# Kernel tuning notes

Hardware: AMD Instinct MI355X
Metric: run time of the kernel (lower is better)

Reference implementation:

```python
import jax, jax.numpy as jnp
import numpy as np

D = 128; H = 8; DH = D // H
N = 50000; B = 8; MAXN = N // B
E = 400000
NG_G = 4; NG_L = 4; NG = NG_G + NG_L
DFF = 2 * D


def _ln(x, eps=1e-5):
    m = x.mean(-1, keepdims=True)
    v = ((x - m) ** 2).mean(-1, keepdims=True)
    return (x - m) * jax.lax.rsqrt(v + eps)


def _mha(q, k, v, in_w, in_b, out_w, out_b):
    # torch nn.MultiheadAttention (batch_first, eval) with packed in_proj
    Bq, Lq, d = q.shape; Lk = k.shape[1]
    wq, wk, wv = jnp.split(in_w, 3, axis=0)
    bq, bk, bv = jnp.split(in_b, 3)
    Q = (q @ wq.T + bq).reshape(Bq, Lq, H, DH).transpose(0, 2, 1, 3)
    K = (k @ wk.T + bk).reshape(Bq, Lk, H, DH).transpose(0, 2, 1, 3)
    V = (v @ wv.T + bv).reshape(Bq, Lk, H, DH).transpose(0, 2, 1, 3)
    A = jax.nn.softmax(jnp.einsum('bhqd,bhkd->bhqk', Q, K) / np.float32(np.sqrt(DH)), axis=-1)
    O = jnp.einsum('bhqk,bhkd->bhqd', A, V).transpose(0, 2, 1, 3).reshape(Bq, Lq, d)
    return O @ out_w.T + out_b, A.mean(axis=1)  # averaged attn weights over heads


def _tconv(x, src, dst, Wq, bq, Wk, bk, Wv, bv, Wskip, bskip, Wbeta):
    # PyG TransformerConv(d, d//H, heads=H, beta=True): edge-wise gather-attend-scatter
    n = x.shape[0]
    q = (x @ Wq.T + bq)[dst].reshape(-1, H, DH)   # [E,H,DH] query at target node
    k = (x @ Wk.T + bk)[src].reshape(-1, H, DH)
    v = (x @ Wv.T + bv)[src].reshape(-1, H, DH)
    logits = (q * k).sum(-1) / np.float32(np.sqrt(DH))  # [E,H]
    m = jax.ops.segment_max(logits, dst, num_segments=n)
    m = jnp.where(jnp.isfinite(m), m, 0.0)
    a = jnp.exp(logits - m[dst])
    s = jax.ops.segment_sum(a, dst, num_segments=n)
    alpha = a / (s[dst] + 1e-16)                  # per-target-node softmax (PyG softmax)
    out = jax.ops.segment_sum(v * alpha[..., None], dst, num_segments=n).reshape(n, D)
    xr = x @ Wskip.T + bskip                      # root weight
    beta = jax.nn.sigmoid(jnp.concatenate([out, xr, out - xr], axis=-1) @ Wbeta.T)
    return beta * xr + (1.0 - beta) * out


def setup_inputs() -> dict:
    key = jax.random.key(0)
    ks = jax.random.split(key, 16)
    w = lambda i, shape, s=0.05: jax.random.normal(ks[i], shape, jnp.float32) * s
    return dict(
        x=w(0, (N, D), 1.0),
        edge_index=jax.random.randint(ks[1], (2, E), 0, N),
        global_h=w(2, (B, NG, D), 1.0),
        batch=jnp.repeat(jnp.arange(B, dtype=jnp.int32), MAXN),  # sorted, even split
        n_global_tokens_global=NG_G,
        n_global_tokens_local=NG_L,
        Wq=w(3, (D, D)), bq=jnp.zeros((D,), jnp.float32),
        Wk=w(4, (D, D)), bk=jnp.zeros((D,), jnp.float32),
        Wv=w(5, (D, D)), bv=jnp.zeros((D,), jnp.float32),
        Wskip=w(6, (D, D)), bskip=jnp.zeros((D,), jnp.float32),
        Wbeta=w(7, (1, 3 * D)),
        ng_in_w=w(8, (3 * D, D)), ng_in_b=jnp.zeros((3 * D,), jnp.float32),
        ng_out_w=w(9, (D, D)), ng_out_b=jnp.zeros((D,), jnp.float32),
        gn_in_w=w(10, (3 * D, D)), gn_in_b=jnp.zeros((3 * D,), jnp.float32),
        gn_out_w=w(11, (D, D)), gn_out_b=jnp.zeros((D,), jnp.float32),
        W1=w(12, (DFF, D)), b1=jnp.zeros((DFF,), jnp.float32),
        W2=w(13, (D, DFF)), b2=jnp.zeros((D,), jnp.float32),
    )


def reference(x, edge_index, global_h, batch, n_global_tokens_global, n_global_tokens_local,
              Wq, bq, Wk, bk, Wv, bv, Wskip, bskip, Wbeta,
              ng_in_w, ng_in_b, ng_out_w, ng_out_b,
              gn_in_w, gn_in_b, gn_out_w, gn_out_b,
              W1, b1, W2, b2):
    src, dst = edge_index[0], edge_index[1]
    h_local = _tconv(x, src, dst, Wq, bq, Wk, bk, Wv, bv, Wskip, bskip, Wbeta)
    x = _ln(x + h_local)
    Bg = global_h.shape[0]
    # to_dense_batch: batch is sorted with equal-size graphs -> mask all True, pure reshape
    dense_x = x.reshape(Bg, -1, D)
    global_out, attn_w = _mha(global_h, dense_x, dense_x, ng_in_w, ng_in_b, ng_out_w, ng_out_b)
    global_h = _ln(global_h + global_out)
    nodes_out, _ = _mha(dense_x, global_h, global_h, gn_in_w, gn_in_b, gn_out_w, gn_out_b)
    dense_x = _ln(dense_x + nodes_out)
    x = dense_x.reshape(-1, D)  # un-scatter (even split -> reshape)
    ff = jax.nn.relu(x @ W1.T + b1) @ W2.T + b2
    x = _ln(x + ff)
    # attention regularization, vectorized over the per-graph python loop
    ls = n_global_tokens_global
    le = ls + n_global_tokens_local
    P = attn_w[:, ls:le, :]                      # [B, K, max_n], all nodes valid
    Pn = P / (P.sum(-1, keepdims=True) + 1e-8)
    G = jnp.einsum('bkn,bmn->bkm', Pn, Pn)       # [B, K, K]
    Kt = le - ls
    off = (G.sum(axis=(1, 2)) - jnp.einsum('bkk->b', G)) / (Kt * Kt - Kt)
    reg = off.mean()
    return x, global_h, reg
```

## Files before the change

kernel.cpp:

```cpp
#include <hip/hip_runtime.h>
#include <math.h>

#define D 128
#define H 8
#define NGT 8
#define LSTOK 4

typedef short bf16x8 __attribute__((ext_vector_type(8)));
typedef float f32x4  __attribute__((ext_vector_type(4)));

__device__ __forceinline__ short f2bf(float f) {
  union { float f; unsigned u; } v; v.f = f;
  unsigned r = v.u + 0x7FFFu + ((v.u >> 16) & 1u);
  return (short)(r >> 16);
}
__device__ __forceinline__ float bf2f(short s) {
  union { unsigned u; float f; } v;
  v.u = ((unsigned)(unsigned short)s) << 16;
  return v.f;
}
__device__ __forceinline__ float4 bf4(bf16x8 v, int lo) {
  return make_float4(bf2f(v[lo]), bf2f(v[lo + 1]), bf2f(v[lo + 2]), bf2f(v[lo + 3]));
}
__device__ __forceinline__ unsigned pk2(float a, float b) {
  return ((unsigned)(unsigned short)f2bf(b) << 16) | (unsigned short)f2bf(a);
}

__device__ __forceinline__ float dot4(float4 a, float4 b) {
  return a.x*b.x + a.y*b.y + a.z*b.z + a.w*b.w;
}
__device__ __forceinline__ float4 scale_madd(float4 a, float sc, float4 v, float p) {
  return make_float4(fmaf(p, v.x, a.x*sc), fmaf(p, v.y, a.y*sc),
                     fmaf(p, v.z, a.z*sc), fmaf(p, v.w, a.w*sc));
}
__device__ __forceinline__ float4 comb4(float4 a, float e1, float4 c, float e2) {
  return make_float4(a.x*e1 + c.x*e2, a.y*e1 + c.y*e2, a.z*e1 + c.z*e2, a.w*e1 + c.w*e2);
}
__device__ __forceinline__ float4 shfl_xor4(float4 v, int off) {
  return make_float4(__shfl_xor(v.x, off), __shfl_xor(v.y, off),
                     __shfl_xor(v.z, off), __shfl_xor(v.w, off));
}

struct CvtArgs {
  const float* s[10];
  short*       d[10];
  int          n[10];
};

__global__ void cvt_weights(CvtArgs a) {
  int which = blockIdx.y;
  const float* s = a.s[which];
  short* d = a.d[which];
  int n = a.n[which];
  int i = (blockIdx.x * 256 + threadIdx.x) * 4;
  if (i + 3 < n) {
    float4 v = *(const float4*)(s + i);
    d[i]     = f2bf(v.x);
    d[i + 1] = f2bf(v.y);
    d[i + 2] = f2bf(v.z);
    d[i + 3] = f2bf(v.w);
  }
}

__global__ void cvt_x(const float* __restrict__ s, short* __restrict__ d, int n) {
  int i = (blockIdx.x * 256 + threadIdx.x) * 8;
  if (i + 7 < n) {
    float4 a = *(const float4*)(s + i);
    float4 b = *(const float4*)(s + i + 4);
    bf16x8 v;
    v[0] = f2bf(a.x); v[1] = f2bf(a.y); v[2] = f2bf(a.z); v[3] = f2bf(a.w);
    v[4] = f2bf(b.x); v[5] = f2bf(b.y); v[6] = f2bf(b.z); v[7] = f2bf(b.w);
    *(bf16x8*)(d + i) = v;
  }
}

__global__ void concat_bias4(const float* __restrict__ b0, const float* __restrict__ b1,
                             const float* __restrict__ b2, const float* __restrict__ b3,
                             float* __restrict__ out) {
  int t = threadIdx.x;
  out[t] = b0[t]; out[128 + t] = b1[t]; out[256 + t] = b2[t]; out[384 + t] = b3[t];
}

#define EPST 72
template<int K>
__global__ void __launch_bounds__(256) gemm_direct(const short* __restrict__ A,
    const short* __restrict__ Wb, const float* __restrict__ bias,
    short* __restrict__ out16, int C16, int s16,
    float* __restrict__ out32, int s32,
    int Nrows, int Ccols, int relu)
{
  __shared__ short eplds[4][64 * EPST];
  const int t = threadIdx.x;
  const int wid = t >> 6, lane = t & 63;
  const int rowBase = blockIdx.x * 128 + (wid >> 1) * 64;
  const int colBase = blockIdx.y * 128 + (wid & 1) * 64;
  const int lrow = lane & 15;
  const int lk = (lane >> 4) * 8;

  f32x4 acc[4][4];
  f32x4 z4 = {0.f, 0.f, 0.f, 0.f};
#pragma unroll
  for (int m = 0; m < 4; m++)
#pragma unroll
    for (int n = 0; n < 4; n++) acc[m][n] = z4;

  const short* ap[4];
#pragma unroll
  for (int m = 0; m < 4; ++m) {
    int ar = rowBase + m * 16 + lrow;
    if (ar >= Nrows) ar = Nrows - 1;
    ap[m] = A + (size_t)ar * K + lk;
  }
  const short* wp[4];
#pragma unroll
  for (int n = 0; n < 4; ++n)
    wp[n] = Wb + (size_t)(colBase + n * 16 + lrow) * K + lk;

#pragma unroll
  for (int kb = 0; kb < K; kb += 32) {
    bf16x8 af[4], bfr[4];
#pragma unroll
    for (int m = 0; m < 4; ++m) af[m] = *(const bf16x8*)(ap[m] + kb);
#pragma unroll
    for (int n = 0; n < 4; ++n) bfr[n] = *(const bf16x8*)(wp[n] + kb);
#pragma unroll
    for (int m = 0; m < 4; ++m)
#pragma unroll
      for (int n = 0; n < 4; ++n)
        acc[m][n] = __builtin_amdgcn_mfma_f32_16x16x32_bf16(af[m], bfr[n], acc[m][n], 0, 0, 0);
  }

  const int ccol = lane & 15;
  const int rquad = (lane >> 4) * 4;
  if (colBase < C16) {
    short* lds = eplds[wid];
#pragma unroll
    for (int n = 0; n < 4; ++n) {
      float bb = bias[colBase + n * 16 + ccol];
      int col = n * 16 + ccol;
#pragma unroll
      for (int m = 0; m < 4; ++m) {
        int r0 = m * 16 + rquad;
#pragma unroll
        for (int r = 0; r < 4; ++r) {
          float v = acc[m][n][r] + bb;
          if (relu) v = fmaxf(v, 0.f);
          lds[(r0 + r) * EPST + col] = f2bf(v);
        }
      }
    }
    const int jr = lane >> 3, jc = lane & 7;
#pragma unroll
    for (int i = 0; i < 8; ++i) {
      int row = i * 8 + jr;
      int gr = rowBase + row;
      if (gr < Nrows) {
        bf16x8 v = *(const bf16x8*)(lds + row * EPST + jc * 8);
        *(bf16x8*)(out16 + (size_t)gr * s16 + colBase + jc * 8) = v;
      }
    }
  } else {
#pragma unroll
    for (int n = 0; n < 4; ++n) {
      int col = colBase + n * 16 + ccol;
      float bb = bias[col];
#pragma unroll
      for (int m = 0; m < 4; ++m) {
        int row0 = rowBase + m * 16 + rquad;
#pragma unroll
        for (int r = 0; r < 4; ++r) {
          int gr = row0 + r;
          if (gr < Nrows) {
            float v = acc[m][n][r] + bb;
            if (relu) v = fmaxf(v, 0.f);
            out32[(size_t)gr * s32 + (col - C16)] = v;
          }
        }
      }
    }
  }
}

__global__ void gemm_small(const float* __restrict__ A, const float* __restrict__ W,
                           const float* __restrict__ bias, float* __restrict__ out, int M)
{
  int r = blockIdx.x;
  int c = threadIdx.x;
  __shared__ float as[128];
  as[c] = A[(size_t)r * 128 + c];
  __syncthreads();
  float acc = bias[c];
  const float* wr = W + (size_t)c * 128;
#pragma unroll 4
  for (int k = 0; k < 128; k++) acc += as[k] * wr[k];
  out[(size_t)r * 128 + c] = acc;
}

__global__ void count_deg(const int* __restrict__ dst, int* __restrict__ deg, int E) {
  int e = blockIdx.x * 256 + threadIdx.x;
  if (e < E) atomicAdd(&deg[dst[e]], 1);
}

__global__ void scan_pass1(const int* __restrict__ deg, int* __restrict__ bsum, int N) {
  int t = threadIdx.x, lane = t & 63, wid = t >> 6;
  int idx = blockIdx.x * 1024 + t * 4;
  int4 v = {0, 0, 0, 0};
  if (idx + 3 < N) v = *(const int4*)(deg + idx);
  else {
    if (idx < N) v.x = deg[idx];
    if (idx + 1 < N) v.y = deg[idx + 1];
    if (idx + 2 < N) v.z = deg[idx + 2];
    if (idx + 3 < N) v.w = deg[idx + 3];
  }
  int s = v.x + v.y + v.z + v.w;
#pragma unroll
  for (int off = 32; off >= 1; off >>= 1) s += __shfl_xor(s, off);
  __shared__ int ws[4];
  if (lane == 0) ws[wid] = s;
  __syncthreads();
  if (t == 0) bsum[blockIdx.x] = ws[0] + ws[1] + ws[2] + ws[3];
}

__global__ void scan_pass2(int* __restrict__ bsum, int SB) {
  __shared__ int sh[1024];
  int t = threadIdx.x;
  sh[t] = (t < SB) ? bsum[t] : 0;
  __syncthreads();
  for (int off = 1; off < 1024; off <<= 1) {
    int v = (t >= off) ? sh[t - off] : 0;
    __syncthreads();
    sh[t] += v;
    __syncthreads();
  }
  if (t < SB) bsum[t] = (t == 0) ? 0 : sh[t - 1];
}

__global__ void scan_pass3(const int* __restrict__ deg, const int* __restrict__ bsum,
                           int* __restrict__ row_start, int* __restrict__ cursor,
                           int N, int E)
{
  int t = threadIdx.x, lane = t & 63, wid = t >> 6;
  int idx = blockIdx.x * 1024 + t * 4;
  int4 v = {0, 0, 0, 0};
  if (idx + 3 < N) v = *(const int4*)(deg + idx);
  else {
    if (idx < N) v.x = deg[idx];
    if (idx + 1 < N) v.y = deg[idx + 1];
    if (idx + 2 < N) v.z = deg[idx + 2];
    if (idx + 3 < N) v.w = deg[idx + 3];
  }
  int ts = v.x + v.y + v.z + v.w;
  int x = ts;
#pragma unroll
  for (int off = 1; off < 64; off <<= 1) {
    int y = __shfl_up(x, off);
    if (lane >= off) x += y;
  }
  __shared__ int ws[4];
  if (lane == 63) ws[wid] = x;
  __syncthreads();
  int woff = 0;
  for (int i = 0; i < wid; i++) woff += ws[i];
  int p = bsum[blockIdx.x] + woff + (x - ts);
  if (idx < N)     { row_start[idx] = p; cursor[idx] = p; }     p += v.x;
  if (idx + 1 < N) { row_start[idx + 1] = p; cursor[idx + 1] = p; } p += v.y;
  if (idx + 2 < N) { row_start[idx + 2] = p; cursor[idx + 2] = p; } p += v.z;
  if (idx + 3 < N) { row_start[idx + 3] = p; cursor[idx + 3] = p; }
  if (blockIdx.x == 0 && t == 0) row_start[N] = E;
}

__global__ void fill_edges(const int* __restrict__ dst, int* __restrict__ cursor,
                           int* __restrict__ edge_list, int E) {
  int e = blockIdx.x * 256 + threadIdx.x;
  if (e < E) {
    int p = atomicAdd(&cursor[dst[e]], 1);
    edge_list[p] = e;
  }
}

__global__ void tconv_attn(const short* __restrict__ qkvb,
                           const int* __restrict__ row_start,
                           const int* __restrict__ edge_list, const int* __restrict__ srcI,
                           float* __restrict__ out, int N)
{
  int gid = blockIdx.x * 256 + threadIdx.x;
  if (gid >= N * H) return;
  int n = gid >> 3, h = gid & 7;
  const short* qp = qkvb + (size_t)n * 384 + h * 16;
  bf16x8 qa = *(const bf16x8*)(qp);
  bf16x8 qb = *(const bf16x8*)(qp + 8);
  float4 q0 = bf4(qa, 0), q1 = bf4(qa, 4), q2 = bf4(qb, 0), q3 = bf4(qb, 4);
  float m = -3.0e38f, s = 0.f;
  float4 a0 = make_float4(0, 0, 0, 0), a1 = a0, a2 = a0, a3 = a0;
  int e1 = row_start[n + 1];
  for (int ei = row_start[n]; ei < e1; ei++) {
    int sn = srcI[edge_list[ei]];
    const short* kp = qkvb + (size_t)sn * 384 + 128 + h * 16;
    bf16x8 k0 = *(const bf16x8*)(kp);
    bf16x8 k1 = *(const bf16x8*)(kp + 8);
    float d = dot4(q0, bf4(k0, 0)) + dot4(q1, bf4(k0, 4))
            + dot4(q2, bf4(k1, 0)) + dot4(q3, bf4(k1, 4));
    d *= 0.25f;
    float mn = fmaxf(m, d);
    float sc = expf(m - mn);
    float p = expf(d - mn);
    bf16x8 v0 = *(const bf16x8*)(kp + 128);
    bf16x8 v1 = *(const bf16x8*)(kp + 136);
    a0 = scale_madd(a0, sc, bf4(v0, 0), p);
    a1 = scale_madd(a1, sc, bf4(v0, 4), p);
    a2 = scale_madd(a2, sc, bf4(v1, 0), p);
    a3 = scale_madd(a3, sc, bf4(v1, 4), p);
    s = s * sc + p;
    m = mn;
  }
  float inv = 1.f / (s + 1e-16f);
  float4* o4 = (float4*)(out + (size_t)n * 128 + h * 16);
  o4[0] = make_float4(a0.x * inv, a0.y * inv, a0.z * inv, a0.w * inv);
  o4[1] = make_float4(a1.x * inv, a1.y * inv, a1.z * inv, a1.w * inv);
  o4[2] = make_float4(a2.x * inv, a2.y * inv, a2.z * inv, a2.w * inv);
  o4[3] = make_float4(a3.x * inv, a3.y * inv, a3.z * inv, a3.w * inv);
}

__global__ void gate_ln(const float* __restrict__ x, const float* __restrict__ att,
                        const float* __restrict__ xr32, const float* __restrict__ Wb,
                        float* __restrict__ x1, short* __restrict__ x1b, int N)
{
  int wid = threadIdx.x >> 6, lane = threadIdx.x & 63;
  int n = blockIdx.x * 4 + wid;
  if (n >= N) return;
  size_t base = (size_t)n * 128 + lane * 2;
  float2 o = *(const float2*)(att + base);
  float2 r = *(const float2*)(xr32 + base);
  float2 xv = *(const float2*)(x + base);
  float2 w0 = *(const float2*)(Wb + lane * 2);
  float2 w1 = *(const float2*)(Wb + 128 + lane * 2);
  float2 w2 = *(const float2*)(Wb + 256 + lane * 2);
  float ts = o.x * w0.x + o.y * w0.y + r.x * w1.x + r.y * w1.y
           + (o.x - r.x) * w2.x + (o.y - r.y) * w2.y;
#pragma unroll
  for (int mm = 32; mm >= 1; mm >>= 1) ts += __shfl_xor(ts, mm);
  float beta = 1.f / (1.f + expf(-ts));
  float2 y;
  y.x = xv.x + beta * r.x + (1.f - beta) * o.x;
  y.y = xv.y + beta * r.y + (1.f - beta) * o.y;
  float sm = y.x + y.y;
#pragma unroll
  for (int mm = 32; mm >= 1; mm >>= 1) sm += __shfl_xor(sm, mm);
  float mean = sm * (1.f / 128.f);
  float dx = y.x - mean, dy = y.y - mean;
  float vs = dx * dx + dy * dy;
#pragma unroll
  for (int mm = 32; mm >= 1; mm >>= 1) vs += __shfl_xor(vs, mm);
  float rstd = rsqrtf(vs * (1.f / 128.f) + 1e-5f);
  float ox = dx * rstd, oy = dy * rstd;
  *(float2*)(x1 + base) = make_float2(ox, oy);
  *(unsigned*)(x1b + base) = pk2(ox, oy);
}

__global__ void ln_add(const float* __restrict__ a, const float* __restrict__ b,
                       float* __restrict__ out, short* __restrict__ out16, int R)
{
  int wid = threadIdx.x >> 6, lane = threadIdx.x & 63;
  int r = blockIdx.x * 4 + wid;
  if (r >= R) return;
  size_t base = (size_t)r * 128 + lane * 2;
  float2 av = *(const float2*)(a + base);
  float2 bv = *(const float2*)(b + base);
  float2 y = make_float2(av.x + bv.x, av.y + bv.y);
  float sm = y.x + y.y;
#pragma unroll
  for (int mm = 32; mm >= 1; mm >>= 1) sm += __shfl_xor(sm, mm);
  float mean = sm * (1.f / 128.f);
  float dx = y.x - mean, dy = y.y - mean;
  float vs = dx * dx + dy * dy;
#pragma unroll
  for (int mm = 32; mm >= 1; mm >>= 1) vs += __shfl_xor(vs, mm);
  float rstd = rsqrtf(vs * (1.f / 128.f) + 1e-5f);
  float ox = dx * rstd, oy = dy * rstd;
  *(float2*)(out + base) = make_float2(ox, oy);
  if (out16) *(unsigned*)(out16 + base) = pk2(ox, oy);
}

__global__ void glob_attn(const float* __restrict__ Qg, const short* __restrict__ kv,
                          float* __restrict__ Og,
                          float* __restrict__ m_gl, float* __restrict__ is_gl, int MAXN)
{
  int blk = blockIdx.x;
  int h = blk & 7, g = (blk >> 3) & 7, b = blk >> 6;
  int lane = threadIdx.x;
  const float4* q4 = (const float4*)(Qg + (size_t)(b * NGT + g) * 128 + h * 16);
  float4 q0 = q4[0], q1 = q4[1], q2 = q4[2], q3 = q4[3];
  float m = -3.0e38f, s = 0.f;
  float4 a0 = make_float4(0, 0, 0, 0), a1 = a0, a2 = a0, a3 = a0;
  for (int n = lane; n < MAXN; n += 64) {
    const short* kp = kv + ((size_t)(b * MAXN + n)) * 256 + h * 16;
    bf16x8 k0 = *(const bf16x8*)(kp);
    bf16x8 k1 = *(const bf16x8*)(kp + 8);
    float d = dot4(q0, bf4(k0, 0)) + dot4(q1, bf4(k0, 4))
            + dot4(q2, bf4(k1, 0)) + dot4(q3, bf4(k1, 4));
    d *= 0.25f;
    float mn = fmaxf(m, d);
    float sc = expf(m - mn);
    float p = expf(d - mn);
    bf16x8 v0 = *(const bf16x8*)(kp + 128);
    bf16x8 v1 = *(const bf16x8*)(kp + 136);
    a0 = scale_madd(a0, sc, bf4(v0, 0), p);
    a1 = scale_madd(a1, sc, bf4(v0, 4), p);
    a2 = scale_madd(a2, sc, bf4(v1, 0), p);
    a3 = scale_madd(a3, sc, bf4(v1, 4), p);
    s = s * sc + p;
    m = mn;
  }
#pragma unroll
  for (int off = 32; off >= 1; off >>= 1) {
    float m2 = __shfl_xor(m, off);
    float s2 = __shfl_xor(s, off);
    float4 c0 = shfl_xor4(a0, off), c1 = shfl_xor4(a1, off);
    float4 c2 = shfl_xor4(a2, off), c3 = shfl_xor4(a3, off);
    float mn = fmaxf(m, m2);
    float e1 = expf(m - mn), e2 = expf(m2 - mn);
    s = s * e1 + s2 * e2;
    a0 = comb4(a0, e1, c0, e2);
    a1 = comb4(a1, e1, c1, e2);
    a2 = comb4(a2, e1, c2, e2);
    a3 = comb4(a3, e1, c3, e2);
    m = mn;
  }
  if (lane == 0) {
    float inv = 1.f / s;
    float4* o4 = (float4*)(Og + (size_t)(b * NGT + g) * 128 + h * 16);
    o4[0] = make_float4(a0.x * inv, a0.y * inv, a0.z * inv, a0.w * inv);
    o4[1] = make_float4(a1.x * inv, a1.y * inv, a1.z * inv, a1.w * inv);
    o4[2] = make_float4(a2.x * inv, a2.y * inv, a2.z * inv, a2.w * inv);
    o4[3] = make_float4(a3.x * inv, a3.y * inv, a3.z * inv, a3.w * inv);
    m_gl[blk] = m;
    is_gl[blk] = inv;
  }
}

__global__ void pker(const float* __restrict__ Qg, const short* __restrict__ kv,
                     const float* __restrict__ m_gl, const float* __restrict__ is_gl,
                     float* __restrict__ P, int MAXN)
{
  int nchunk = (MAXN + 255) >> 8;
  int b = blockIdx.x / nchunk;
  int ch = blockIdx.x % nchunk;
  __shared__ float qs[4 * 128];
  __shared__ float ms[32], iss[32];
  for (int i = threadIdx.x; i < 512; i += 256)
    qs[i] = Qg[(size_t)(b * NGT + LSTOK) * 128 + i];
  if (threadIdx.x < 32) {
    int g = threadIdx.x >> 3, h = threadIdx.x & 7;
    ms[threadIdx.x]  = m_gl[(b * NGT + LSTOK + g) * H + h];
    iss[threadIdx.x] = is_gl[(b * NGT + LSTOK + g) * H + h];
  }
  __syncthreads();
  int n = ch * 256 + threadIdx.x;
  if (n >= MAXN) return;
  float acc[4] = {0.f, 0.f, 0.f, 0.f};
  const short* kbase = kv + ((size_t)(b * MAXN + n)) * 256;
  for (int h = 0; h < H; h++) {
    bf16x8 ka = *(const bf16x8*)(kbase + h * 16);
    bf16x8 kb = *(const bf16x8*)(kbase + h * 16 + 8);
    float4 k0 = bf4(ka, 0), k1 = bf4(ka, 4), k2 = bf4(kb, 0), k3 = bf4(kb, 4);
#pragma unroll
    for (int g = 0; g < 4; g++) {
      const float4* qp = (const float4*)(qs + g * 128 + h * 16);
      float d = dot4(k0, qp[0]) + dot4(k1, qp[1]) + dot4(k2, qp[2]) + dot4(k3, qp[3]);
      d *= 0.25f;
      acc[g] += expf(d - ms[g * 8 + h]) * iss[g * 8 + h];
    }
  }
#pragma unroll
  for (int g = 0; g < 4; g++)
    P[(size_t)(b * 4 + g) * MAXN + n] = acc[g] * 0.125f;
}

__global__ void regk(const float* __restrict__ P, float* __restrict__ offb, int MAXN)
{
  int b = blockIdx.x;
  int t = threadIdx.x;
  float v[10];
#pragma unroll
  for (int i = 0; i < 10; i++) v[i] = 0.f;
  for (int n = t; n < MAXN; n += 256) {
    float p0 = P[(size_t)(b * 4 + 0) * MAXN + n];
    float p1 = P[(size_t)(b * 4 + 1) * MAXN + n];
    float p2 = P[(size_t)(b * 4 + 2) * MAXN + n];
    float p3 = P[(size_t)(b * 4 + 3) * MAXN + n];
    v[0] += p0; v[1] += p1; v[2] += p2; v[3] += p3;
    v[4] += p0 * p1; v[5] += p0 * p2; v[6] += p0 * p3;
    v[7] += p1 * p2; v[8] += p1 * p3; v[9] += p2 * p3;
  }
#pragma unroll
  for (int i = 0; i < 10; i++) {
    float x = v[i];
#pragma unroll
    for (int mm = 32; mm >= 1; mm >>= 1) x += __shfl_xor(x, mm);
    v[i] = x;
  }
  __shared__ float red[4][10];
  int wid = t >> 6, lane = t & 63;
  if (lane == 0)
    for (int i = 0; i < 10; i++) red[wid][i] = v[i];
  __syncthreads();
  if (t == 0) {
    float r[10];
    for (int i = 0; i < 10; i++) r[i] = red[0][i] + red[1][i] + red[2][i] + red[3][i];
    float r0 = r[0] + 1e-8f, r1 = r[1] + 1e-8f, r2 = r[2] + 1e-8f, r3 = r[3] + 1e-8f;
    float off = 2.f * (r[4] / (r0 * r1) + r[5] / (r0 * r2) + r[6] / (r0 * r3)
                     + r[7] / (r1 * r2) + r[8] / (r1 * r3) + r[9] / (r2 * r3));
    offb[b] = off * (1.f / 12.f);
  }
}

__global__ void regfin(const float* __restrict__ offb, float* __restrict__ out) {
  if (threadIdx.x == 0 && blockIdx.x == 0) {
    float s = 0.f;
    for (int i = 0; i < 8; i++) s += offb[i];
    *out = s * (1.f / 8.f);
  }
}

__global__ void node_attn(const short* __restrict__ Qn, const float* __restrict__ Kg,
                          const float* __restrict__ Vg, short* __restrict__ On,
                          int N, int MAXN)
{
  __shared__ float kg[2][NGT * 128];
  __shared__ float vg[2][NGT * 128];
  int n0 = blockIdx.x * 32;
  int b0 = n0 / MAXN;
  int nlast = n0 + 31; if (nlast >= N) nlast = N - 1;
  int bLast = nlast / MAXN;
  int nb = (bLast != b0) ? 2 : 1;
  for (int bi = 0; bi < nb; ++bi) {
    size_t gb = (size_t)((b0 + bi) * NGT) * 128;
    int i = threadIdx.x * 4;
    *(float4*)&kg[bi][i] = *(const float4*)(Kg + gb + i);
    *(float4*)&vg[bi][i] = *(const float4*)(Vg + gb + i);
  }
  __syncthreads();
  int n = n0 + (threadIdx.x >> 3), h = threadIdx.x & 7;
  if (n >= N) return;
  int bi = (n / MAXN) - b0;
  const short* qp = Qn + (size_t)n * 128 + h * 16;
  bf16x8 qa = *(const bf16x8*)(qp);
  bf16x8 qb = *(const bf16x8*)(qp + 8);
  float4 q0 = bf4(qa, 0), q1 = bf4(qa, 4), q2 = bf4(qb, 0), q3 = bf4(qb, 4);
  float l[NGT];
  float mx = -3.0e38f;
#pragma unroll
  for (int tk = 0; tk < NGT; tk++) {
    const float4* k4 = (const float4*)(&kg[bi][tk * 128 + h * 16]);
    float d = dot4(q0, k4[0]) + dot4(q1, k4[1]) + dot4(q2, k4[2]) + dot4(q3, k4[3]);
    l[tk] = d * 0.25f;
    mx = fmaxf(mx, l[tk]);
  }
  float s = 0.f;
#pragma unroll
  for (int tk = 0; tk < NGT; tk++) { l[tk] = expf(l[tk] - mx); s += l[tk]; }
  float inv = 1.f / s;
  float4 a0 = make_float4(0, 0, 0, 0), a1 = a0, a2 = a0, a3 = a0;
#pragma unroll
  for (int tk = 0; tk < NGT; tk++) {
    float p = l[tk] * inv;
    const float4* v4 = (const float4*)(&vg[bi][tk * 128 + h * 16]);
    a0 = scale_madd(a0, 1.f, v4[0], p);
    a1 = scale_madd(a1, 1.f, v4[1], p);
    a2 = scale_madd(a2, 1.f, v4[2], p);
    a3 = scale_madd(a3, 1.f, v4[3], p);
  }
  unsigned* o = (unsigned*)(On + (size_t)n * 128 + h * 16);
  o[0] = pk2(a0.x, a0.y); o[1] = pk2(a0.z, a0.w);
  o[2] = pk2(a1.x, a1.y); o[3] = pk2(a1.z, a1.w);
  o[4] = pk2(a2.x, a2.y); o[5] = pk2(a2.z, a2.w);
  o[6] = pk2(a3.x, a3.y); o[7] = pk2(a3.z, a3.w);
}

extern "C" void kernel_launch(void* const* d_in, const int* in_sizes, int n_in,
                              void* d_out, int out_size, void* d_ws, size_t ws_size,
                              hipStream_t stream)
{
  const float* x     = (const float*)d_in[0];
  const int*   ei    = (const int*)d_in[1];
  const float* gh    = (const float*)d_in[2];
  const float* Wq    = (const float*)d_in[6];
  const float* bqv   = (const float*)d_in[7];
  const float* Wk    = (const float*)d_in[8];
  const float* bkv   = (const float*)d_in[9];
  const float* Wv    = (const float*)d_in[10];
  const float* bvv   = (const float*)d_in[11];
  const float* Wsk   = (const float*)d_in[12];
  const float* bsk   = (const float*)d_in[13];
  const float* Wbeta = (const float*)d_in[14];
  const float* ngw   = (const float*)d_in[15];
  const float* ngb   = (const float*)d_in[16];
  const float* ngow  = (const float*)d_in[17];
  const float* ngob  = (const float*)d_in[18];
  const float* gnw   = (const float*)d_in[19];
  const float* gnb   = (const float*)d_in[20];
  const float* gnow  = (const float*)d_in[21];
  const float* gnob  = (const float*)d_in[22];
  const float* W1    = (const float*)d_in[23];
  const float* b1v   = (const float*)d_in[24];
  const float* W2    = (const float*)d_in[25];
  const float* b2v   = (const float*)d_in[26];

  const int N    = in_sizes[0] / D;
  const int E    = in_sizes[1] / 2;
  const int Bb   = 8;
  const int MAXN = N / Bb;

  const int* srcI = ei;
  const int* dstI = ei + E;

  size_t NF = (size_t)N;
  size_t ND = NF * D;
  float* fw = (float*)d_ws;
  short* qkvb = (short*)fw;
  short* kv16 = qkvb;
  short* ff1b = qkvb;
  float* xr32 = fw + NF * 192;
  short* Qnb  = (short*)xr32;
  short* Onb  = (short*)(xr32 + NF * 64);
  float* ff2o = xr32;
  float* x1   = fw + NF * 320;
  short* x1b  = (short*)(fw + NF * 448);
  float* misc = fw + NF * 512;
  float* Qg    = misc;
  float* Og    = Qg + 8192;
  float* gout  = Og + 8192;
  float* Kg    = gout + 8192;
  float* Vg    = Kg + 8192;
  float* m_gl  = Vg + 8192;
  float* is_gl = m_gl + 512;
  float* Pbuf  = is_gl + 512;
  float* offb  = Pbuf + (size_t)Bb * 4 * MAXN;
  float* bias512 = offb + 16;
  int* deg       = (int*)(bias512 + 512);
  int* row_start = deg + N;
  int* cursor    = row_start + N + 1;
  int* bsum      = cursor + N;
  int* edge_list = bsum + 1024;
  short* wbase = (short*)((((uintptr_t)(edge_list + E)) + 15) & ~(uintptr_t)15);
  short* cWq  = wbase;
  short* cWk  = cWq  + 16384;
  short* cWv  = cWk  + 16384;
  short* cWsk = cWv  + 16384;
  short* cNgK = cWsk + 16384;
  short* cNgV = cNgK + 16384;
  short* cGnQ = cNgV + 16384;
  short* cGnO = cGnQ + 16384;
  short* cW1  = cGnO + 16384;
  short* cW2  = cW1  + 32768;
  short* xb   = cW2  + 32768;

  float* outx   = (float*)d_out;
  float* outgh  = outx + ND;
  float* outreg = outgh + (size_t)Bb * NGT * D;
  float* wa     = outx;

  const int GXM = (N + 127) / 128;
  const int SB  = (N + 1023) / 1024;
  dim3 blk256(256);

  CvtArgs ca;
  ca.s[0] = Wq;   ca.d[0] = cWq;  ca.n[0] = 16384;
  ca.s[1] = Wk;   ca.d[1] = cWk;  ca.n[1] = 16384;
  ca.s[2] = Wv;   ca.d[2] = cWv;  ca.n[2] = 16384;
  ca.s[3] = Wsk;  ca.d[3] = cWsk; ca.n[3] = 16384;
  ca.s[4] = ngw + 128 * 128; ca.d[4] = cNgK; ca.n[4] = 16384;
  ca.s[5] = ngw + 256 * 128; ca.d[5] = cNgV; ca.n[5] = 16384;
  ca.s[6] = gnw;  ca.d[6] = cGnQ; ca.n[6] = 16384;
  ca.s[7] = gnow; ca.d[7] = cGnO; ca.n[7] = 16384;
  ca.s[8] = W1;   ca.d[8] = cW1;  ca.n[8] = 32768;
  ca.s[9] = W2;   ca.d[9] = cW2;  ca.n[9] = 32768;
  cvt_weights<<<dim3(32, 10), blk256, 0, stream>>>(ca);
  concat_bias4<<<dim3(1), dim3(128), 0, stream>>>(bqv, bkv, bvv, bsk, bias512);
  cvt_x<<<dim3((N * 128 / 8 + 255) / 256), blk256, 0, stream>>>(x, xb, N * 128);

  hipMemsetAsync(deg, 0, (size_t)N * sizeof(int), stream);
  count_deg<<<dim3((E + 255) / 256), blk256, 0, stream>>>(dstI, deg, E);
  scan_pass1<<<dim3(SB), blk256, 0, stream>>>(deg, bsum, N);
  scan_pass2<<<dim3(1), dim3(1024), 0, stream>>>(bsum, SB);
  scan_pass3<<<dim3(SB), blk256, 0, stream>>>(deg, bsum, row_start, cursor, N, E);
  fill_edges<<<dim3((E + 255) / 256), blk256, 0, stream>>>(dstI, cursor, edge_list, E);

  gemm_direct<128><<<dim3(GXM, 4), blk256, 0, stream>>>(xb, cWq, bias512,
                                                        qkvb, 384, 384, xr32, 128,
                                                        N, 512, 0);

  tconv_attn<<<dim3((N * H + 255) / 256), blk256, 0, stream>>>(qkvb, row_start, edge_list, srcI, wa, N);
  gate_ln<<<dim3((N + 3) / 4), blk256, 0, stream>>>(x, wa, xr32, Wbeta, x1, x1b, N);

  gemm_direct<128><<<dim3(GXM, 2), blk256, 0, stream>>>(x1b, cNgK, ngb + 128,
                                                        kv16, 256, 256, nullptr, 0,
                                                        N, 256, 0);
  gemm_small<<<dim3(64), dim3(128), 0, stream>>>(gh, ngw, ngb, Qg, 64);
  glob_attn<<<dim3(512), dim3(64), 0, stream>>>(Qg, kv16, Og, m_gl, is_gl, MAXN);
  pker<<<dim3(8 * ((MAXN + 255) / 256)), blk256, 0, stream>>>(Qg, kv16, m_gl, is_gl, Pbuf, MAXN);
  regk<<<dim3(8), blk256, 0, stream>>>(Pbuf, offb, MAXN);
  regfin<<<dim3(1), dim3(64), 0, stream>>>(offb, outreg);

  gemm_small<<<dim3(64), dim3(128), 0, stream>>>(Og, ngow, ngob, gout, 64);
  ln_add<<<dim3(16), blk256, 0, stream>>>(gh, gout, outgh, nullptr, 64);

  gemm_small<<<dim3(64), dim3(128), 0, stream>>>(outgh, gnw + 128 * 128, gnb + 128, Kg, 64);
  gemm_small<<<dim3(64), dim3(128), 0, stream>>>(outgh, gnw + 256 * 128, gnb + 256, Vg, 64);
  gemm_direct<128><<<dim3(GXM, 1), blk256, 0, stream>>>(x1b, cGnQ, gnb,
                                                        Qnb, 128, 128, nullptr, 0,
                                                        N, 128, 0);
  node_attn<<<dim3((N + 31) / 32), blk256, 0, stream>>>(Qnb, Kg, Vg, Onb, N, MAXN);
  gemm_direct<128><<<dim3(GXM, 1), blk256, 0, stream>>>(Onb, cGnO, gnob,
                                                        nullptr, 0, 0, wa, 128,
                                                        N, 128, 0);
  ln_add<<<dim3((N + 3) / 4), blk256, 0, stream>>>(x1, wa, x1, x1b, N);

  gemm_direct<128><<<dim3(GXM, 2), blk256, 0, stream>>>(x1b, cW1, b1v,
                                                        ff1b, 256, 256, nullptr, 0,
                                                        N, 256, 1);
  gemm_direct<256><<<dim3(GXM, 1), blk256, 0, stream>>>(ff1b, cW2, b2v,
                                                        nullptr, 0, 0, ff2o, 128,
                                                        N, 128, 0);
  ln_add<<<dim3((N + 3) / 4), blk256, 0, stream>>>(x1, ff2o, outx, nullptr, N);
}
```

Baseline: 419.2 us.

## Split global attention over node chunks and reuse stored logits for regularizer

The global-token attention kernel is split into NCH=4 node chunks per (batch, token, head), so it runs 2048 single-wave blocks instead of 512, and a merge kernel combines the partial max, sum and accumulator values. The local-token logits are written out during the first pass, so the regularizer kernel reads them instead of reloading K and recomputing the dot products. The cost is an extra launch, extra global writes and reads for the logits buffer (4*H*B*MAXN floats), and an enlarged workspace.

```diff
diff --git a/kernel.cpp b/kernel.cpp
--- a/kernel.cpp
+++ b/kernel.cpp
@@ -5,6 +5,7 @@
 #define H 8
 #define NGT 8
 #define LSTOK 4
+#define NCH 4
 
 typedef short bf16x8 __attribute__((ext_vector_type(8)));
 typedef float f32x4  __attribute__((ext_vector_type(4)));
@@ -381,24 +382,31 @@
   if (out16) *(unsigned*)(out16 + base) = pk2(ox, oy);
 }
 
-__global__ void glob_attn(const float* __restrict__ Qg, const short* __restrict__ kv,
-                          float* __restrict__ Og,
-                          float* __restrict__ m_gl, float* __restrict__ is_gl, int MAXN)
+__global__ void glob_part(const float* __restrict__ Qg, const short* __restrict__ kv,
+                          float* __restrict__ Plog,
+                          float* __restrict__ pm, float* __restrict__ ps,
+                          float* __restrict__ pacc, int MAXN)
 {
   int blk = blockIdx.x;
+  int ch = blockIdx.y;
   int h = blk & 7, g = (blk >> 3) & 7, b = blk >> 6;
   int lane = threadIdx.x;
   const float4* q4 = (const float4*)(Qg + (size_t)(b * NGT + g) * 128 + h * 16);
   float4 q0 = q4[0], q1 = q4[1], q2 = q4[2], q3 = q4[3];
+  int chunk = (MAXN + NCH - 1) / NCH;
+  int n0 = ch * chunk;
+  int n1 = n0 + chunk; if (n1 > MAXN) n1 = MAXN;
+  float* plrow = (g >= LSTOK) ? Plog + (((size_t)(b * 4 + g - LSTOK)) * H + h) * MAXN : nullptr;
   float m = -3.0e38f, s = 0.f;
   float4 a0 = make_float4(0, 0, 0, 0), a1 = a0, a2 = a0, a3 = a0;
-  for (int n = lane; n < MAXN; n += 64) {
+  for (int n = n0 + lane; n < n1; n += 64) {
     const short* kp = kv + ((size_t)(b * MAXN + n)) * 256 + h * 16;
     bf16x8 k0 = *(const bf16x8*)(kp);
     bf16x8 k1 = *(const bf16x8*)(kp + 8);
     float d = dot4(q0, bf4(k0, 0)) + dot4(q1, bf4(k0, 4))
             + dot4(q2, bf4(k1, 0)) + dot4(q3, bf4(k1, 4));
     d *= 0.25f;
+    if (plrow) plrow[n] = d;
     float mn = fmaxf(m, d);
     float sc = expf(m - mn);
     float p = expf(d - mn);
@@ -427,53 +435,60 @@
     m = mn;
   }
   if (lane == 0) {
-    float inv = 1.f / s;
-    float4* o4 = (float4*)(Og + (size_t)(b * NGT + g) * 128 + h * 16);
-    o4[0] = make_float4(a0.x * inv, a0.y * inv, a0.z * inv, a0.w * inv);
-    o4[1] = make_float4(a1.x * inv, a1.y * inv, a1.z * inv, a1.w * inv);
-    o4[2] = make_float4(a2.x * inv, a2.y * inv, a2.z * inv, a2.w * inv);
-    o4[3] = make_float4(a3.x * inv, a3.y * inv, a3.z * inv, a3.w * inv);
-    m_gl[blk] = m;
-    is_gl[blk] = inv;
-  }
-}
-
-__global__ void pker(const float* __restrict__ Qg, const short* __restrict__ kv,
-                     const float* __restrict__ m_gl, const float* __restrict__ is_gl,
-                     float* __restrict__ P, int MAXN)
-{
-  int nchunk = (MAXN + 255) >> 8;
-  int b = blockIdx.x / nchunk;
-  int ch = blockIdx.x % nchunk;
-  __shared__ float qs[4 * 128];
+    int pi = blk * NCH + ch;
+    pm[pi] = m; ps[pi] = s;
+    float4* pa = (float4*)(pacc + (size_t)pi * 16);
+    pa[0] = a0; pa[1] = a1; pa[2] = a2; pa[3] = a3;
+  }
+}
+
+__global__ void glob_merge(const float* __restrict__ pm, const float* __restrict__ ps,
+                           const float* __restrict__ pacc, float* __restrict__ Og,
+                           float* __restrict__ m_gl, float* __restrict__ is_gl)
+{
+  int blk = blockIdx.x;
+  int lane = threadIdx.x;
+  float m = -3.0e38f;
+#pragma unroll
+  for (int c = 0; c < NCH; ++c) m = fmaxf(m, pm[blk * NCH + c]);
+  float s = 0.f;
+#pragma unroll
+  for (int c = 0; c < NCH; ++c) s += ps[blk * NCH + c] * expf(pm[blk * NCH + c] - m);
+  if (lane < 16) {
+    float a = 0.f;
+#pragma unroll
+    for (int c = 0; c < NCH; ++c)
+      a += pacc[(size_t)(blk * NCH + c) * 16 + lane] * expf(pm[blk * NCH + c] - m);
+    int h = blk & 7, g = (blk >> 3) & 7, b = blk >> 6;
+    Og[(size_t)(b * NGT + g) * 128 + h * 16 + lane] = a / s;
+  }
+  if (lane == 0) { m_gl[blk] = m; is_gl[blk] = 1.f / s; }
+}
+
+__global__ void pker2(const float* __restrict__ Plog,
+                      const float* __restrict__ m_gl, const float* __restrict__ is_gl,
+                      float* __restrict__ P, int MAXN)
+{
+  int b = blockIdx.y;
   __shared__ float ms[32], iss[32];
-  for (int i = threadIdx.x; i < 512; i += 256)
-    qs[i] = Qg[(size_t)(b * NGT + LSTOK) * 128 + i];
   if (threadIdx.x < 32) {
     int g = threadIdx.x >> 3, h = threadIdx.x & 7;
     ms[threadIdx.x]  = m_gl[(b * NGT + LSTOK + g) * H + h];
     iss[threadIdx.x] = is_gl[(b * NGT + LSTOK + g) * H + h];
   }
   __syncthreads();
-  int n = ch * 256 + threadIdx.x;
+  int n = blockIdx.x * 256 + threadIdx.x;
   if (n >= MAXN) return;
-  float acc[4] = {0.f, 0.f, 0.f, 0.f};
-  const short* kbase = kv + ((size_t)(b * MAXN + n)) * 256;
-  for (int h = 0; h < H; h++) {
-    bf16x8 ka = *(const bf16x8*)(kbase + h * 16);
-    bf16x8 kb = *(const bf16x8*)(kbase + h * 16 + 8);
-    float4 k0 = bf4(ka, 0), k1 = bf4(ka, 4), k2 = bf4(kb, 0), k3 = bf4(kb, 4);
-#pragma unroll
-    for (int g = 0; g < 4; g++) {
-      const float4* qp = (const float4*)(qs + g * 128 + h * 16);
-      float d = dot4(k0, qp[0]) + dot4(k1, qp[1]) + dot4(k2, qp[2]) + dot4(k3, qp[3]);
-      d *= 0.25f;
-      acc[g] += expf(d - ms[g * 8 + h]) * iss[g * 8 + h];
+#pragma unroll
+  for (int g = 0; g < 4; g++) {
+    float acc = 0.f;
+#pragma unroll
+    for (int h = 0; h < H; h++) {
+      float l = Plog[(((size_t)(b * 4 + g)) * H + h) * MAXN + n];
+      acc += expf(l - ms[g * 8 + h]) * iss[g * 8 + h];
     }
-  }
-#pragma unroll
-  for (int g = 0; g < 4; g++)
-    P[(size_t)(b * 4 + g) * MAXN + n] = acc[g] * 0.125f;
+    P[(size_t)(b * 4 + g) * MAXN + n] = acc * 0.125f;
+  }
 }
 
 __global__ void regk(const float* __restrict__ P, float* __restrict__ offb, int MAXN)
@@ -637,7 +652,11 @@
   float* Pbuf  = is_gl + 512;
   float* offb  = Pbuf + (size_t)Bb * 4 * MAXN;
   float* bias512 = offb + 16;
-  int* deg       = (int*)(bias512 + 512);
+  float* Plog  = bias512 + 512;
+  float* pm    = Plog + (size_t)4 * H * Bb * MAXN;
+  float* ps    = pm + 512 * NCH;
+  float* pacc  = ps + 512 * NCH;
+  int* deg       = (int*)(pacc + 512 * NCH * 16);
   int* row_start = deg + N;
   int* cursor    = row_start + N + 1;
   int* bsum      = cursor + N;
@@ -697,8 +716,9 @@
                                                         kv16, 256, 256, nullptr, 0,
                                                         N, 256, 0);
   gemm_small<<<dim3(64), dim3(128), 0, stream>>>(gh, ngw, ngb, Qg, 64);
-  glob_attn<<<dim3(512), dim3(64), 0, stream>>>(Qg, kv16, Og, m_gl, is_gl, MAXN);
-  pker<<<dim3(8 * ((MAXN + 255) / 256)), blk256, 0, stream>>>(Qg, kv16, m_gl, is_gl, Pbuf, MAXN);
+  glob_part<<<dim3(512, NCH), dim3(64), 0, stream>>>(Qg, kv16, Plog, pm, ps, pacc, MAXN);
+  glob_merge<<<dim3(512), dim3(64), 0, stream>>>(pm, ps, pacc, Og, m_gl, is_gl);
+  pker2<<<dim3((MAXN + 255) / 256, 8), blk256, 0, stream>>>(Plog, m_gl, is_gl, Pbuf, MAXN);
   regk<<<dim3(8), blk256, 0, stream>>>(Pbuf, offb, MAXN);
   regfin<<<dim3(1), dim3(64), 0, stream>>>(offb, outreg);
 
```

Result: faster. 399.5 us (-4.7%).
